# Kernel tuning notes

Measured on AMD Instinct MI355X. Metric: run time of the kernel, lower is better.

Reference implementation:

```python
import jax, jax.numpy as jnp
import numpy as np

B, S, D = 4, 4096, 128

def setup_inputs() -> dict:
    key = jax.random.key(0)
    ks = jax.random.split(key, 7)
    s = 1.0 / np.sqrt(D)
    return {
        "x": jax.random.normal(ks[0], (B, S, D), dtype=jnp.float32),
        "Wq": jax.random.normal(ks[1], (D, D), dtype=jnp.float32) * s,
        "bq": jax.random.normal(ks[2], (D,), dtype=jnp.float32) * s,
        "Wk": jax.random.normal(ks[3], (D, D), dtype=jnp.float32) * s,
        "bk": jax.random.normal(ks[4], (D,), dtype=jnp.float32) * s,
        "Wv": jax.random.normal(ks[5], (D, D), dtype=jnp.float32) * s,
        "bv": jax.random.normal(ks[6], (D,), dtype=jnp.float32) * s,
    }

def reference(x, Wq, bq, Wk, bk, Wv, bv):
    # Linear projections (torch Linear: x @ W^T + b)
    Q = jnp.einsum('bsd,ed->bse', x, Wq) + bq
    K = jnp.einsum('bsd,ed->bse', x, Wk) + bk
    V = jnp.einsum('bsd,ed->bse', x, Wv) + bv
    scale = jnp.sqrt(jnp.asarray(x.shape[-1], dtype=x.dtype))
    scores = jnp.einsum('bqd,bkd->bqk', Q, K) / scale  # [B,S,S]
    weights = jax.nn.softmax(scores, axis=-1)
    return jnp.einsum('bqk,bkd->bqd', weights, V)
```

## Files before the change

kernel.cpp:

```cpp
#include <hip/hip_runtime.h>
#include <hip/hip_bf16.h>
#include <stdint.h>

#define NB 4
#define NS 4096
#define ND 128
#define KVBLK 32
#define NT32 (NS / KVBLK)
#define QBLK 128

typedef __attribute__((ext_vector_type(8))) short short8;
typedef __attribute__((ext_vector_type(4))) float f32x4;
typedef __attribute__((ext_vector_type(16))) float f32x16;
typedef __attribute__((ext_vector_type(2))) int i32x2;
typedef _Float16 f16;

#define QSCALE 0.12751744f
#define SOFF 12.0f

__device__ __forceinline__ unsigned short f2bfu(float f) {
  __hip_bfloat16 h = __float2bfloat16(f);
  union { __hip_bfloat16 h; unsigned short u; } c; c.h = h; return c.u;
}
__device__ __forceinline__ uint32_t pack2bf(float lo, float hi) {
  return (uint32_t)f2bfu(lo) | ((uint32_t)f2bfu(hi) << 16);
}

__device__ __forceinline__ void gl_lds16(const void* g, void* l) {
  __builtin_amdgcn_global_load_lds(
      (const __attribute__((address_space(1))) uint32_t*)g,
      (__attribute__((address_space(3))) uint32_t*)l, 16, 0, 0);
}

#define MFMA16(a, b, c) __builtin_amdgcn_mfma_f32_16x16x32_bf16((a), (b), (c), 0, 0, 0)
#define MFMA32(a, b, c) __builtin_amdgcn_mfma_f32_32x32x16_bf16((a), (b), (c), 0, 0, 0)

#if __has_builtin(__builtin_amdgcn_permlane32_swap)
#define PLSWAP(lo_, hi_)                                                        \
  { i32x2 r_ = __builtin_amdgcn_permlane32_swap((int)(lo_), (int)(hi_), false,  \
                                                false);                         \
    lo_ = (uint32_t)r_[0]; hi_ = (uint32_t)r_[1]; }
#else
#define PLSWAP(lo_, hi_)                                                        \
  { uint32_t sA_ = hi ? (lo_) : (hi_);                                          \
    uint32_t rA_ = (uint32_t)__shfl_xor((int)sA_, 32, 64);                      \
    uint32_t nl_ = hi ? rA_ : (lo_);                                            \
    uint32_t nh_ = hi ? (hi_) : rA_;                                            \
    lo_ = nl_; hi_ = nh_; }
#endif

__global__ __launch_bounds__(256) void proj_kernel(
    const float* __restrict__ x,
    const float* __restrict__ Wq, const float* __restrict__ bq,
    const float* __restrict__ Wk, const float* __restrict__ bk,
    const float* __restrict__ Wv, const float* __restrict__ bv,
    unsigned short* __restrict__ Qo, unsigned short* __restrict__ Ko,
    unsigned short* __restrict__ Vt)
{
  __shared__ unsigned short XsTt[128 * 72];
  __shared__ unsigned short Ws[128 * 128];

  const int tile  = blockIdx.x;
  const int b     = blockIdx.y;
  const int which = blockIdx.z;

  const float* W    = (which == 0) ? Wq : (which == 1) ? Wk : Wv;
  const float* bias = (which == 0) ? bq : (which == 1) ? bk : bv;

  const int t = threadIdx.x;
  const int wave = t >> 6, lane = t & 63;
  const int lr = lane & 15, lg = lane >> 4;

  const float* xb = x + ((size_t)b * NS + (size_t)tile * 64) * ND;

#pragma unroll
  for (int c = 0; c < 4; ++c) {
    int eo = (c * 256 + t) * 8;
    int row = eo >> 7, col = eo & 127;
    const float4* s = (const float4*)(xb + row * ND + col);
    float4 v0 = s[0], v1 = s[1];
    short8 o;
    o[0] = (short)f2bfu(v0.x); o[1] = (short)f2bfu(v0.y);
    o[2] = (short)f2bfu(v0.z); o[3] = (short)f2bfu(v0.w);
    o[4] = (short)f2bfu(v1.x); o[5] = (short)f2bfu(v1.y);
    o[6] = (short)f2bfu(v1.z); o[7] = (short)f2bfu(v1.w);
    int ba = (row * 256 + col * 2) ^ ((row & 7) << 4);
    *(short8*)((char*)XsTt + ba) = o;
  }
#pragma unroll
  for (int c = 0; c < 8; ++c) {
    int eo = (c * 256 + t) * 8;
    int row = eo >> 7, col = eo & 127;
    const float4* s = (const float4*)(W + row * ND + col);
    float4 v0 = s[0], v1 = s[1];
    short8 o;
    o[0] = (short)f2bfu(v0.x); o[1] = (short)f2bfu(v0.y);
    o[2] = (short)f2bfu(v0.z); o[3] = (short)f2bfu(v0.w);
    o[4] = (short)f2bfu(v1.x); o[5] = (short)f2bfu(v1.y);
    o[6] = (short)f2bfu(v1.z); o[7] = (short)f2bfu(v1.w);
    int ba = (row * 256 + col * 2) ^ ((row & 7) << 4);
    *(short8*)((char*)Ws + ba) = o;
  }
  __syncthreads();

  short8 af[4];
#pragma unroll
  for (int kk = 0; kk < 4; ++kk) {
    int row = wave * 16 + lr;
    int ba = (row * 256 + kk * 64 + lg * 16) ^ ((row & 7) << 4);
    af[kk] = *(const short8*)((const char*)XsTt + ba);
  }
  f32x4 acc[8] = {};
#pragma unroll
  for (int kk = 0; kk < 4; ++kk) {
#pragma unroll
    for (int nf = 0; nf < 8; ++nf) {
      int n = nf * 16 + lr;
      int ba = (n * 256 + kk * 64 + lg * 16) ^ ((n & 7) << 4);
      short8 bf = *(const short8*)((const char*)Ws + ba);
      acc[nf] = MFMA16(af[kk], bf, acc[nf]);
    }
  }

  if (which < 2) {
    unsigned short* Out = (which == 0) ? Qo : Ko;
    const float sc = (which == 0) ? QSCALE : 1.0f;
#pragma unroll
    for (int nf = 0; nf < 8; ++nf) {
      float bb = bias[nf * 16 + lr];
#pragma unroll
      for (int r = 0; r < 4; ++r) {
        float v = (acc[nf][r] + bb) * sc;
        int row = tile * 64 + wave * 16 + lg * 4 + r;
        Out[((size_t)b * NS + row) * ND + nf * 16 + lr] = f2bfu(v);
      }
    }
  } else {
    __syncthreads();
    unsigned short* Tt = XsTt;
#pragma unroll
    for (int nf = 0; nf < 8; ++nf) {
      float bb = bias[nf * 16 + lr];
#pragma unroll
      for (int r = 0; r < 4; ++r) {
        int e = nf * 16 + lr;
        int sl = wave * 16 + lg * 4 + r;
        Tt[e * 72 + sl] = f2bfu(acc[nf][r] + bb);
      }
    }
    __syncthreads();
    int e = t >> 1, off = (t & 1) * 32;
    const short8* src = (const short8*)(Tt + e * 72 + off);
    short8* dst = (short8*)(Vt + ((size_t)b * ND + e) * NS + (size_t)tile * 64 + off);
#pragma unroll
    for (int i = 0; i < 4; ++i) dst[i] = src[i];
  }
}

__global__ __launch_bounds__(256, 3) void attn_kernel(
    const unsigned short* __restrict__ Q, const unsigned short* __restrict__ K,
    const unsigned short* __restrict__ Vt, f16* __restrict__ OP,
    float* __restrict__ Lp, int nchunk)
{
  __shared__ char smem[32768];

  const int Lid = blockIdx.x;
  const int ngroups = NB * nchunk;
  int g, qt;
  if ((ngroups & 7) == 0) {
    int xcd = Lid & 7, s2 = Lid >> 3;
    qt = s2 & 31;
    g = xcd * (ngroups >> 3) + (s2 >> 5);
  } else { qt = Lid & 31; g = Lid >> 5; }
  const int b = g / nchunk, c = g - b * nchunk;

  const int cbase = NT32 / nchunk, crem = NT32 - cbase * nchunk;
  const int tstart = c * cbase + (c < crem ? c : crem);
  const int ntpc = cbase + (c < crem ? 1 : 0);

  const int t = threadIdx.x, wave = t >> 6, lane = t & 63;
  const int lq = lane & 31, hi = lane >> 5;

  const int qrow = qt * QBLK + wave * 32 + lq;
  short8 qf[8];
  const unsigned short* Qb = Q + ((size_t)b * NS + qrow) * ND;
#pragma unroll
  for (int kt = 0; kt < 8; ++kt) qf[kt] = *(const short8*)(Qb + kt * 16 + hi * 8);

  const char* Kbase = (const char*)(K + (size_t)b * NS * ND) +
                      (size_t)tstart * (KVBLK * ND * 2);
  const char* Vbase = (const char*)(Vt + (size_t)b * ND * NS) +
                      (size_t)tstart * (KVBLK * 2);

  auto stage = [&](int p, int tt) {
    const char* ksrc = Kbase + (size_t)tt * 8192;
    const char* vsrc = Vbase + (size_t)tt * 64;
    char* kd = smem + p * 8192;
    char* vd = smem + 16384 + p * 8192;
#pragma unroll
    for (int j = 0; j < 2; ++j) {
      int y = (wave * 2 + j) * 1024 + lane * 16;
      int so = y ^ (((y >> 8) & 15) << 4);
      gl_lds16(ksrc + so, kd + y);
      int d = y >> 6, col = y & 63;
      int cx = col ^ (((d >> 1) & 3) << 4);
      gl_lds16(vsrc + (size_t)d * (NS * 2) + cx, vd + y);
    }
  };

  f32x16 oacc[4] = {};
  float l = 0.f;

  stage(0, 0);
  __syncthreads();

  for (int tt = 0; tt < ntpc; ++tt) {
    const int p = tt & 1;
    const char* kb = smem + p * 8192;
    const char* vb = smem + 16384 + p * 8192;
    if (tt + 1 < ntpc) stage(p ^ 1, tt + 1);

    f32x16 s0 = {};
    const int ksw = (lq & 15) << 4;
    __builtin_amdgcn_s_setprio(1);
#pragma unroll
    for (int kt = 0; kt < 8; ++kt) {
      int co = (kt * 32 + hi * 16) ^ ksw;
      short8 k0 = *(const short8*)(kb + lq * 256 + co);
      s0 = MFMA32(k0, qf[kt], s0);
    }
    __builtin_amdgcn_s_setprio(0);

    float u0 = 0.f, u1 = 0.f, u2 = 0.f, u3 = 0.f;
#pragma unroll
    for (int r = 0; r < 16; r += 4) {
      s0[r]     = exp2f(s0[r] - SOFF);
      s0[r + 1] = exp2f(s0[r + 1] - SOFF);
      s0[r + 2] = exp2f(s0[r + 2] - SOFF);
      s0[r + 3] = exp2f(s0[r + 3] - SOFF);
      u0 += s0[r]; u1 += s0[r + 1]; u2 += s0[r + 2]; u3 += s0[r + 3];
    }
    l += (u0 + u1) + (u2 + u3);

    uint32_t pk[8];
#pragma unroll
    for (int i = 0; i < 8; ++i) pk[i] = pack2bf(s0[2 * i], s0[2 * i + 1]);
    short8 pfrag[2];
#pragma unroll
    for (int kt2 = 0; kt2 < 2; ++kt2) {
      uint32_t e0 = pk[4 * kt2 + 0], e1 = pk[4 * kt2 + 1];
      uint32_t e2 = pk[4 * kt2 + 2], e3 = pk[4 * kt2 + 3];
      PLSWAP(e0, e2);
      PLSWAP(e1, e3);
      union { uint32_t u[4]; short8 s; } pf;
      pf.u[0] = e0; pf.u[1] = e1; pf.u[2] = e2; pf.u[3] = e3;
      pfrag[kt2] = pf.s;
    }

    const int vsw = ((lq >> 1) & 3) << 4;
    __builtin_amdgcn_s_setprio(1);
#pragma unroll
    for (int dt = 0; dt < 4; ++dt) {
      int rowb = (dt * 32 + lq) * 64;
#pragma unroll
      for (int kt2 = 0; kt2 < 2; ++kt2) {
        int co = (kt2 * 32 + hi * 16) ^ vsw;
        short8 vf = *(const short8*)(vb + rowb + co);
        oacc[dt] = MFMA32(vf, pfrag[kt2], oacc[dt]);
      }
    }
    __builtin_amdgcn_s_setprio(0);

    __syncthreads();
  }

  float lt = l + __shfl_xor(l, 32, 64);
  f16* OPb = OP + ((size_t)(c * NB + b) * ND) * NS + qrow;
#pragma unroll
  for (int dt = 0; dt < 4; ++dt)
#pragma unroll
    for (int r = 0; r < 16; ++r) {
      int d = dt * 32 + (r & 3) + 8 * (r >> 2) + 4 * hi;
      OPb[(size_t)d * NS] = (f16)oacc[dt][r];
    }
  if (hi == 0)
    Lp[(size_t)(c * NB + b) * NS + qrow] = lt;
}

template <int NC>
__global__ __launch_bounds__(256) void combine_kernel(
    const f16* __restrict__ OP, const float* __restrict__ Lp,
    float* __restrict__ Out)
{
  __shared__ float Linv[32];
  __shared__ float LT[32][129];

  const int qtile = blockIdx.x, b = blockIdx.y;
  const int t = threadIdx.x;

  if (t < 32) {
    size_t qg = (size_t)qtile * 32 + t;
    float L = 0.f;
#pragma unroll
    for (int cc = 0; cc < NC; ++cc)
      L += Lp[(size_t)(cc * NB + b) * NS + qg];
    Linv[t] = 1.0f / L;
  }
  __syncthreads();

  const int so = (t & 3) * 8;
  const int dl = t >> 2;
  const size_t sbase = (size_t)qtile * 32 + so;
#pragma unroll
  for (int dblk = 0; dblk < 2; ++dblk) {
    int d = dblk * 64 + dl;
    float a0 = 0, a1 = 0, a2 = 0, a3 = 0, a4 = 0, a5 = 0, a6 = 0, a7 = 0;
#pragma unroll
    for (int cc = 0; cc < NC; ++cc) {
      const f16* src = OP + ((size_t)(cc * NB + b) * ND + d) * NS + sbase;
      short8 v = *(const short8*)src;
      union { short s; f16 h; } u;
      u.s = v[0]; a0 += (float)u.h;
      u.s = v[1]; a1 += (float)u.h;
      u.s = v[2]; a2 += (float)u.h;
      u.s = v[3]; a3 += (float)u.h;
      u.s = v[4]; a4 += (float)u.h;
      u.s = v[5]; a5 += (float)u.h;
      u.s = v[6]; a6 += (float)u.h;
      u.s = v[7]; a7 += (float)u.h;
    }
    LT[so + 0][d] = a0 * Linv[so + 0]; LT[so + 1][d] = a1 * Linv[so + 1];
    LT[so + 2][d] = a2 * Linv[so + 2]; LT[so + 3][d] = a3 * Linv[so + 3];
    LT[so + 4][d] = a4 * Linv[so + 4]; LT[so + 5][d] = a5 * Linv[so + 5];
    LT[so + 6][d] = a6 * Linv[so + 6]; LT[so + 7][d] = a7 * Linv[so + 7];
  }
  __syncthreads();

  const int d2 = t & 127, qh = t >> 7;
  float* Ob = Out + ((size_t)b * NS + (size_t)qtile * 32) * ND;
#pragma unroll 8
  for (int pass = 0; pass < 16; ++pass) {
    int qq = pass * 2 + qh;
    Ob[(size_t)qq * ND + d2] = LT[qq][d2];
  }
}

extern "C" void kernel_launch(void* const* d_in, const int* in_sizes, int n_in,
                              void* d_out, int out_size, void* d_ws, size_t ws_size,
                              hipStream_t stream) {
  const float* x  = (const float*)d_in[0];
  const float* Wq = (const float*)d_in[1];
  const float* bq = (const float*)d_in[2];
  const float* Wk = (const float*)d_in[3];
  const float* bk = (const float*)d_in[4];
  const float* Wv = (const float*)d_in[5];
  const float* bv = (const float*)d_in[6];

  const size_t elems = (size_t)NB * NS * ND;
  char* base = (char*)d_ws;
  unsigned short* Qw  = (unsigned short*)base;
  unsigned short* Kw  = Qw + elems;
  unsigned short* Vtw = Kw + elems;
  char* region2 = base + 3 * elems * 2;

  int nchunk = 6;
  for (;;) {
    size_t need = 3 * elems * 2 +
                  (size_t)nchunk * (elems * 2 + (size_t)NB * NS * 4);
    if (need <= ws_size || nchunk == 1) break;
    nchunk = (nchunk == 6) ? 4 : nchunk >> 1;
  }

  f16* OPw = (f16*)region2;
  float* Lpw = (float*)(region2 + (size_t)nchunk * elems * 2);

  proj_kernel<<<dim3(NS / 64, NB, 3), 256, 0, stream>>>(
      x, Wq, bq, Wk, bk, Wv, bv, Qw, Kw, Vtw);

  attn_kernel<<<dim3(32 * NB * nchunk), 256, 0, stream>>>(
      Qw, Kw, Vtw, OPw, Lpw, nchunk);

  dim3 cgrid(NS / 32, NB);
  switch (nchunk) {
    case 6: combine_kernel<6><<<cgrid, 256, 0, stream>>>(OPw, Lpw, (float*)d_out); break;
    case 4: combine_kernel<4><<<cgrid, 256, 0, stream>>>(OPw, Lpw, (float*)d_out); break;
    case 2: combine_kernel<2><<<cgrid, 256, 0, stream>>>(OPw, Lpw, (float*)d_out); break;
    default: combine_kernel<1><<<cgrid, 256, 0, stream>>>(OPw, Lpw, (float*)d_out); break;
  }
}
```

Measured before the change: 71.63 us.

## Store partial attention outputs row-major to drop combine-stage transpose

The attention kernel now writes its fp16 partial output in [q][d] order with packed 64-bit stores, replacing the scattered per-element stores with stride NS. The combine kernel then reads contiguous d-runs per query and writes float4 outputs directly, removing the shared-memory transpose buffer and a barrier. This trades strided global stores for 8-byte partial-line stores in the attention epilogue.

```diff
diff --git a/kernel.cpp b/kernel.cpp
--- a/kernel.cpp
+++ b/kernel.cpp
@@ -275,13 +275,18 @@
   }
 
   float lt = l + __shfl_xor(l, 32, 64);
-  f16* OPb = OP + ((size_t)(c * NB + b) * ND) * NS + qrow;
+  f16* OPq = OP + ((size_t)(c * NB + b) * NS + qrow) * ND;
 #pragma unroll
   for (int dt = 0; dt < 4; ++dt)
 #pragma unroll
-    for (int r = 0; r < 16; ++r) {
-      int d = dt * 32 + (r & 3) + 8 * (r >> 2) + 4 * hi;
-      OPb[(size_t)d * NS] = (f16)oacc[dt][r];
+    for (int rq = 0; rq < 4; ++rq) {
+      int d0 = dt * 32 + 8 * rq + 4 * hi;
+      union { f16 h[4]; uint64_t u; } pkv;
+      pkv.h[0] = (f16)oacc[dt][rq * 4 + 0];
+      pkv.h[1] = (f16)oacc[dt][rq * 4 + 1];
+      pkv.h[2] = (f16)oacc[dt][rq * 4 + 2];
+      pkv.h[3] = (f16)oacc[dt][rq * 4 + 3];
+      *(uint64_t*)(OPq + d0) = pkv.u;
     }
   if (hi == 0)
     Lp[(size_t)(c * NB + b) * NS + qrow] = lt;
@@ -293,7 +298,6 @@
     float* __restrict__ Out)
 {
   __shared__ float Linv[32];
-  __shared__ float LT[32][129];
 
   const int qtile = blockIdx.x, b = blockIdx.y;
   const int t = threadIdx.x;
@@ -308,16 +312,16 @@
   }
   __syncthreads();
 
-  const int so = (t & 3) * 8;
-  const int dl = t >> 2;
-  const size_t sbase = (size_t)qtile * 32 + so;
-#pragma unroll
-  for (int dblk = 0; dblk < 2; ++dblk) {
-    int d = dblk * 64 + dl;
+  const int dr = (t & 15) * 8;
+  const int qr = t >> 4;
+#pragma unroll
+  for (int pass = 0; pass < 2; ++pass) {
+    int q = pass * 16 + qr;
+    size_t qg = (size_t)qtile * 32 + q;
     float a0 = 0, a1 = 0, a2 = 0, a3 = 0, a4 = 0, a5 = 0, a6 = 0, a7 = 0;
 #pragma unroll
     for (int cc = 0; cc < NC; ++cc) {
-      const f16* src = OP + ((size_t)(cc * NB + b) * ND + d) * NS + sbase;
+      const f16* src = OP + ((size_t)(cc * NB + b) * NS + qg) * ND + dr;
       short8 v = *(const short8*)src;
       union { short s; f16 h; } u;
       u.s = v[0]; a0 += (float)u.h;
@@ -329,19 +333,12 @@
       u.s = v[6]; a6 += (float)u.h;
       u.s = v[7]; a7 += (float)u.h;
     }
-    LT[so + 0][d] = a0 * Linv[so + 0]; LT[so + 1][d] = a1 * Linv[so + 1];
-    LT[so + 2][d] = a2 * Linv[so + 2]; LT[so + 3][d] = a3 * Linv[so + 3];
-    LT[so + 4][d] = a4 * Linv[so + 4]; LT[so + 5][d] = a5 * Linv[so + 5];
-    LT[so + 6][d] = a6 * Linv[so + 6]; LT[so + 7][d] = a7 * Linv[so + 7];
-  }
-  __syncthreads();
-
-  const int d2 = t & 127, qh = t >> 7;
-  float* Ob = Out + ((size_t)b * NS + (size_t)qtile * 32) * ND;
-#pragma unroll 8
-  for (int pass = 0; pass < 16; ++pass) {
-    int qq = pass * 2 + qh;
-    Ob[(size_t)qq * ND + d2] = LT[qq][d2];
+    float inv = Linv[q];
+    float* dst = Out + ((size_t)b * NS + qg) * ND + dr;
+    float4 w0 = {a0 * inv, a1 * inv, a2 * inv, a3 * inv};
+    float4 w1 = {a4 * inv, a5 * inv, a6 * inv, a7 * inv};
+    *(float4*)dst = w0;
+    *(float4*)(dst + 4) = w1;
   }
 }
 
```

Result: no change. 70.45 us (-1.6%).
